# Kernel tuning notes

Hardware: AMD Instinct MI355X
Metric: run time of the kernel (lower is better)

## Reference

```python
import jax, jax.numpy as jnp
import numpy as np

NU = 100000  # user nodes
NI = 100000  # item nodes
D_IN = 128
D_OUT = 128
E = 800000   # edges per canonical etype


def setup_inputs() -> dict:
    key = jax.random.key(0)
    ks = jax.random.split(key, 14)
    s = 1.0 / np.sqrt(D_IN)
    return {
        "feat_user": jax.random.normal(ks[0], (NU, D_IN), jnp.float32),
        "feat_item": jax.random.normal(ks[1], (NI, D_IN), jnp.float32),
        "W_follows": jax.random.normal(ks[2], (D_OUT, D_IN), jnp.float32) * s,
        "b_follows": jax.random.normal(ks[3], (D_OUT,), jnp.float32) * s,
        "W_rates": jax.random.normal(ks[4], (D_OUT, D_IN), jnp.float32) * s,
        "b_rates": jax.random.normal(ks[5], (D_OUT,), jnp.float32) * s,
        "W_ratedby": jax.random.normal(ks[6], (D_OUT, D_IN), jnp.float32) * s,
        "b_ratedby": jax.random.normal(ks[7], (D_OUT,), jnp.float32) * s,
        "src_follows": jax.random.randint(ks[8], (E,), 0, NU),
        "dst_follows": jax.random.randint(ks[9], (E,), 0, NU),
        "src_rates": jax.random.randint(ks[10], (E,), 0, NU),
        "dst_rates": jax.random.randint(ks[11], (E,), 0, NI),
        "src_ratedby": jax.random.randint(ks[12], (E,), 0, NI),
        "dst_ratedby": jax.random.randint(ks[13], (E,), 0, NU),
    }


def _mean_agg(Wh, src, dst, n_dst):
    # gather transformed src features per edge, segment-mean over dst
    msg = Wh[src]  # [E, D_OUT]
    s = jax.ops.segment_sum(msg, dst, num_segments=n_dst)
    cnt = jax.ops.segment_sum(jnp.ones((dst.shape[0],), Wh.dtype), dst,
                              num_segments=n_dst)
    return s / jnp.maximum(cnt, 1.0)[:, None]  # zero-degree -> 0, like DGL


def reference(feat_user, feat_item, W_follows, b_follows, W_rates, b_rates,
              W_ratedby, b_ratedby, src_follows, dst_follows, src_rates,
              dst_rates, src_ratedby, dst_ratedby):
    # per-etype linear transform of source node features (Wh)
    Wh_f = feat_user @ W_follows.T + b_follows    # user -> user
    Wh_r = feat_user @ W_rates.T + b_rates        # user -> item
    Wh_rb = feat_item @ W_ratedby.T + b_ratedby   # item -> user
    # copy_u/mean per etype, then 'sum' combine across etypes per dst ntype
    h_user = (_mean_agg(Wh_f, src_follows, dst_follows, NU)
              + _mean_agg(Wh_rb, src_ratedby, dst_ratedby, NU))
    h_item = _mean_agg(Wh_r, src_rates, dst_rates, NI)
    return (h_user, h_item)
```

## Files before the change

### kernel.cpp

```cpp
#include <hip/hip_runtime.h>

#define NU 100000
#define NI 100000
#define DF 128
#define CAP 32
#define BCAP 768
#define NBKT 1600
#define CHUNK 4096

typedef __attribute__((ext_vector_type(8))) short bf16x8;
typedef __attribute__((ext_vector_type(4))) float f32x4;

__device__ __forceinline__ unsigned short f2bf(float f) {
    unsigned u = __float_as_uint(f);
    return (unsigned short)((u + 0x7fffu + ((u >> 16) & 1u)) >> 16);
}
__device__ __forceinline__ float bflo(unsigned v) { return __uint_as_float(v << 16); }
__device__ __forceinline__ float bfhi(unsigned v) { return __uint_as_float(v & 0xffff0000u); }

__global__ void wcvt_kernel(const float* __restrict__ W0,
                            const float* __restrict__ W1,
                            const float* __restrict__ W2,
                            unsigned short* __restrict__ out,
                            int* __restrict__ bcnt)
{
    const int i = blockIdx.x * 256 + threadIdx.x;
    if (i < 3 * 16384) {
        const float* src = (i < 16384) ? W0 : ((i < 32768) ? W1 : W2);
        out[i] = f2bf(src[i & 16383]);
    }
    if (i < 3 * NBKT * 16) bcnt[i] = 0;
}

__device__ __forceinline__ void load_afrag(const float* __restrict__ A,
                                           int row0, int q, int n, int M,
                                           bf16x8 afrag[2][4])
{
#pragma unroll
    for (int t = 0; t < 2; ++t) {
        const int rr = min(row0 + t * 16 + n, M - 1);
        const float* ap = A + (size_t)rr * DF + q * 8;
#pragma unroll
        for (int s = 0; s < 4; ++s) {
            const float4 f0 = *(const float4*)(ap + s * 32);
            const float4 f1 = *(const float4*)(ap + s * 32 + 4);
            bf16x8 fr;
            fr[0] = (short)f2bf(f0.x); fr[1] = (short)f2bf(f0.y);
            fr[2] = (short)f2bf(f0.z); fr[3] = (short)f2bf(f0.w);
            fr[4] = (short)f2bf(f1.x); fr[5] = (short)f2bf(f1.y);
            fr[6] = (short)f2bf(f1.z); fr[7] = (short)f2bf(f1.w);
            afrag[t][s] = fr;
        }
    }
}

__device__ __forceinline__ void mat_pass(const bf16x8 afrag[2][4],
                                         const unsigned short* __restrict__ Wbp,
                                         const float* __restrict__ bias,
                                         unsigned short* __restrict__ ot,
                                         int wv, int q, int n)
{
#pragma unroll 1
    for (int c = 0; c < 8; ++c) {
        const unsigned short* wp = Wbp + (size_t)(c * 16 + n) * DF + q * 8;
        bf16x8 bfrag[4];
#pragma unroll
        for (int s = 0; s < 4; ++s)
            bfrag[s] = *(const bf16x8*)(wp + s * 32);

        f32x4 acc0 = {0.f, 0.f, 0.f, 0.f};
        f32x4 acc1 = {0.f, 0.f, 0.f, 0.f};
#pragma unroll
        for (int s = 0; s < 4; ++s) {
            acc0 = __builtin_amdgcn_mfma_f32_16x16x32_bf16(afrag[0][s], bfrag[s], acc0, 0, 0, 0);
            acc1 = __builtin_amdgcn_mfma_f32_16x16x32_bf16(afrag[1][s], bfrag[s], acc1, 0, 0, 0);
        }

        const float bv = bias[c * 16 + n];
        const int col2 = (c * 16 + n) * 2;
#pragma unroll
        for (int i = 0; i < 4; ++i) {
            const int r0 = wv * 32 + q * 4 + i;
            const int swz = (r0 & 7) << 4;
            *(unsigned short*)((char*)ot + ((r0 * 256 + col2) ^ swz))       = f2bf(acc0[i] + bv);
            *(unsigned short*)((char*)ot + (((r0 + 16) * 256 + col2) ^ swz)) = f2bf(acc1[i] + bv);
        }
    }
}

__device__ __forceinline__ void flush_tile(const unsigned short* __restrict__ ot,
                                           unsigned short* __restrict__ Wh,
                                           int rowbase, int M, int tid)
{
    __syncthreads();
#pragma unroll
    for (int it = 0; it < 8; ++it) {
        const int chunk = it * 256 + tid;
        const int row = chunk >> 4;
        const int lbyte = chunk * 16;
        const uint4 v = *(const uint4*)((const char*)ot + (lbyte ^ ((row & 7) << 4)));
        if (rowbase + row < M)
            *(uint4*)((char*)Wh + (size_t)(rowbase + row) * 256 + (lbyte & 255)) = v;
    }
    __syncthreads();
}

__global__ __launch_bounds__(256)
void gemm3_kernel(const float* __restrict__ Au, const float* __restrict__ Ai,
                  const unsigned short* __restrict__ Wb,
                  const float* __restrict__ b_f, const float* __restrict__ b_r,
                  const float* __restrict__ b_rb,
                  unsigned short* __restrict__ Wh_f,
                  unsigned short* __restrict__ Wh_r,
                  unsigned short* __restrict__ Wh_rb, int M)
{
    __shared__ unsigned short ot[128 * 128];
    const int tid  = threadIdx.x;
    const int lane = tid & 63;
    const int wv   = tid >> 6;
    const int q    = lane >> 4;
    const int n    = lane & 15;
    const int row0 = blockIdx.x * 128 + wv * 32;

    bf16x8 afrag[2][4];
    load_afrag(Au, row0, q, n, M, afrag);
    mat_pass(afrag, Wb,             b_f, ot, wv, q, n);
    flush_tile(ot, Wh_f, blockIdx.x * 128, M, tid);
    mat_pass(afrag, Wb + 2 * 16384, b_r, ot, wv, q, n);
    flush_tile(ot, Wh_r, blockIdx.x * 128, M, tid);
    load_afrag(Ai, row0, q, n, M, afrag);
    mat_pass(afrag, Wb + 16384,     b_rb, ot, wv, q, n);
    flush_tile(ot, Wh_rb, blockIdx.x * 128, M, tid);
}

__global__ __launch_bounds__(256)
void bin3_kernel(const int* __restrict__ src0, const int* __restrict__ dst0, int n0, int nb0,
                 const int* __restrict__ src1, const int* __restrict__ dst1, int n1, int nb1,
                 const int* __restrict__ src2, const int* __restrict__ dst2, int n2,
                 int* __restrict__ bcnt, unsigned* __restrict__ pairs)
{
    __shared__ int hist[NBKT];
    const int tid = threadIdx.x;
    int b = blockIdx.x, e;
    const int* src; const int* dst; int n;
    if (b < nb0)            { e = 0; src = src0; dst = dst0; n = n0; }
    else if (b < nb0 + nb1) { b -= nb0; e = 1; src = src1; dst = dst1; n = n1; }
    else                    { b -= nb0 + nb1; e = 2; src = src2; dst = dst2; n = n2; }
    const int base = b * CHUNK;
    int* bc = bcnt + e * NBKT * 16;
    unsigned* pr = pairs + (size_t)e * NBKT * BCAP;

    for (int j = tid; j < NBKT; j += 256) hist[j] = 0;
    __syncthreads();

    unsigned pk[16];
    int meta[16];
#pragma unroll
    for (int k = 0; k < 16; ++k) {
        const int i = base + k * 256 + tid;
        if (i < n) {
            const unsigned d = (unsigned)dst[i];
            const unsigned s = (unsigned)src[i];
            pk[k] = (s << 6) | (d & 63u);
            const int p = atomicAdd(&hist[d >> 6], 1);
            meta[k] = (int)((d >> 6) << 16) | p;
        } else meta[k] = -1;
    }
    __syncthreads();
    for (int j = tid; j < NBKT; j += 256) {
        const int c = hist[j];
        hist[j] = (c > 0) ? atomicAdd(&bc[j * 16], c) : 0;
    }
    __syncthreads();
#pragma unroll
    for (int k = 0; k < 16; ++k) {
        if (meta[k] >= 0) {
            const int bkt = meta[k] >> 16;
            const int p = hist[bkt] + (meta[k] & 0xffff);
            if (p < BCAP) pr[(size_t)bkt * BCAP + p] = pk[k];
        }
    }
}

__device__ __forceinline__ void accum8(const uint4 u, float acc[8]) {
    acc[0] += bflo(u.x); acc[1] += bfhi(u.x);
    acc[2] += bflo(u.y); acc[3] += bfhi(u.y);
    acc[4] += bflo(u.z); acc[5] += bfhi(u.z);
    acc[6] += bflo(u.w); acc[7] += bfhi(u.w);
}

__device__ __forceinline__ void gather_q(const unsigned short* __restrict__ Wh,
                                         const unsigned* __restrict__ sl,
                                         int d, int qh, int c16, float acc[8])
{
    for (int j = 0; j < d; j += 8) {
        const int e0 = j + qh, e1 = j + 2 + qh, e2 = j + 4 + qh, e3 = j + 6 + qh;
        uint4 u0 = {0,0,0,0}, u1 = {0,0,0,0}, u2 = {0,0,0,0}, u3 = {0,0,0,0};
        if (e0 < d) u0 = *((const uint4*)(Wh + (size_t)sl[e0] * DF) + c16);
        if (e1 < d) u1 = *((const uint4*)(Wh + (size_t)sl[e1] * DF) + c16);
        if (e2 < d) u2 = *((const uint4*)(Wh + (size_t)sl[e2] * DF) + c16);
        if (e3 < d) u3 = *((const uint4*)(Wh + (size_t)sl[e3] * DF) + c16);
        accum8(u0, acc); accum8(u1, acc);
        accum8(u2, acc); accum8(u3, acc);
    }
}

__global__ __launch_bounds__(256, 8)
void bagg_kernel(const unsigned short* __restrict__ Wh_f,
                 const unsigned short* __restrict__ Wh_rb,
                 const unsigned short* __restrict__ Wh_r,
                 const int* __restrict__ bcnt, const unsigned* __restrict__ pairs,
                 float* __restrict__ out_user, float* __restrict__ out_item)
{
    __shared__ int cntA[64], cntB[64];
    __shared__ unsigned slotA[64 * CAP], slotB[64 * CAP];
    const int tid = threadIdx.x;
    const bool user = (blockIdx.x & 1) == 0;
    const int bkt = blockIdx.x >> 1;

    if (tid < 64) { cntA[tid] = 0; cntB[tid] = 0; }
    __syncthreads();

    const int wv = tid >> 6, lane = tid & 63;
    const int c16 = lane & 15;
    const int qh = (lane >> 4) & 1;
    const int h = lane >> 5;

    if (user) {
        const int nf  = min(bcnt[0 * NBKT * 16 + bkt * 16], BCAP);
        const int nrb = min(bcnt[1 * NBKT * 16 + bkt * 16], BCAP);
        const unsigned* prf  = pairs + (size_t)bkt * BCAP;
        const unsigned* prrb = pairs + (size_t)NBKT * BCAP + (size_t)bkt * BCAP;
        for (int i = tid; i < nf; i += 256) {
            const unsigned v = prf[i];
            const int dl = v & 63;
            const int p = atomicAdd(&cntA[dl], 1);
            if (p < CAP) slotA[dl * CAP + p] = v >> 6;
        }
        for (int i = tid; i < nrb; i += 256) {
            const unsigned v = prrb[i];
            const int dl = v & 63;
            const int p = atomicAdd(&cntB[dl], 1);
            if (p < CAP) slotB[dl * CAP + p] = v >> 6;
        }
        __syncthreads();

        for (int t = 0; t < 8; ++t) {
            const int dl = wv * 16 + t * 2 + h;
            const int node = bkt * 64 + dl;
            const int degf  = cntA[dl];
            const int degrb = cntB[dl];
            const int df  = min(degf, CAP);
            const int drb = min(degrb, CAP);

            float acc[8];
#pragma unroll
            for (int k = 0; k < 8; ++k) acc[k] = 0.f;
            gather_q(Wh_f, &slotA[dl * CAP], df, qh, c16, acc);
            const float invf = degf > 0 ? 1.f / (float)degf : 0.f;
            float res[8];
#pragma unroll
            for (int k = 0; k < 8; ++k) { res[k] = acc[k] * invf; acc[k] = 0.f; }

            gather_q(Wh_rb, &slotB[dl * CAP], drb, qh, c16, acc);
            const float invrb = degrb > 0 ? 1.f / (float)degrb : 0.f;
#pragma unroll
            for (int k = 0; k < 8; ++k) {
                res[k] += acc[k] * invrb;
                res[k] += __shfl_xor(res[k], 16, 64);
            }
            if (!(lane & 16) && node < NU) {
                float* op = out_user + (size_t)node * DF + c16 * 8;
                float4 o0 = {res[0], res[1], res[2], res[3]};
                float4 o1 = {res[4], res[5], res[6], res[7]};
                *(float4*)op = o0;
                *((float4*)op + 1) = o1;
            }
        }
    } else {
        const int nr = min(bcnt[2 * NBKT * 16 + bkt * 16], BCAP);
        const unsigned* prr = pairs + 2 * (size_t)NBKT * BCAP + (size_t)bkt * BCAP;
        for (int i = tid; i < nr; i += 256) {
            const unsigned v = prr[i];
            const int dl = v & 63;
            const int p = atomicAdd(&cntA[dl], 1);
            if (p < CAP) slotA[dl * CAP + p] = v >> 6;
        }
        __syncthreads();

        for (int t = 0; t < 8; ++t) {
            const int dl = wv * 16 + t * 2 + h;
            const int node = bkt * 64 + dl;
            const int degr = cntA[dl];
            const int dr = min(degr, CAP);

            float acc[8];
#pragma unroll
            for (int k = 0; k < 8; ++k) acc[k] = 0.f;
            gather_q(Wh_r, &slotA[dl * CAP], dr, qh, c16, acc);
            const float invr = degr > 0 ? 1.f / (float)degr : 0.f;
            float res[8];
#pragma unroll
            for (int k = 0; k < 8; ++k) {
                res[k] = acc[k] * invr;
                res[k] += __shfl_xor(res[k], 16, 64);
            }
            if (!(lane & 16) && node < NI) {
                float* op = out_item + (size_t)node * DF + c16 * 8;
                float4 o0 = {res[0], res[1], res[2], res[3]};
                float4 o1 = {res[4], res[5], res[6], res[7]};
                *(float4*)op = o0;
                *((float4*)op + 1) = o1;
            }
        }
    }
}

extern "C" void kernel_launch(void* const* d_in, const int* in_sizes, int n_in,
                              void* d_out, int out_size, void* d_ws,
                              size_t ws_size, hipStream_t stream)
{
    const float* feat_user = (const float*)d_in[0];
    const float* feat_item = (const float*)d_in[1];
    const float* W_f  = (const float*)d_in[2];
    const float* b_f  = (const float*)d_in[3];
    const float* W_r  = (const float*)d_in[4];
    const float* b_r  = (const float*)d_in[5];
    const float* W_rb = (const float*)d_in[6];
    const float* b_rb = (const float*)d_in[7];
    const int* src_f  = (const int*)d_in[8];
    const int* dst_f  = (const int*)d_in[9];
    const int* src_r  = (const int*)d_in[10];
    const int* dst_r  = (const int*)d_in[11];
    const int* src_rb = (const int*)d_in[12];
    const int* dst_rb = (const int*)d_in[13];
    const int Ef  = in_sizes[8];
    const int Er  = in_sizes[10];
    const int Erb = in_sizes[12];

    float* out_user = (float*)d_out;
    float* out_item = (float*)d_out + (size_t)NU * DF;

    char* p = (char*)d_ws;
    unsigned short* Wh_f  = (unsigned short*)p;  p += (size_t)NU * DF * 2;
    unsigned short* Wh_rb = (unsigned short*)p;  p += (size_t)NI * DF * 2;
    unsigned short* Wh_r  = (unsigned short*)p;  p += (size_t)NU * DF * 2;
    unsigned* pairs = (unsigned*)p;  p += 3 * (size_t)NBKT * BCAP * 4;
    int* bcnt = (int*)p;             p += 3 * (size_t)NBKT * 16 * 4;
    unsigned short* Wb = (unsigned short*)p;

    wcvt_kernel<<<300, 256, 0, stream>>>(W_f, W_rb, W_r, Wb, bcnt);

    gemm3_kernel<<<(NU + 127) / 128, 256, 0, stream>>>(
        feat_user, feat_item, Wb, b_f, b_r, b_rb, Wh_f, Wh_r, Wh_rb, NU);

    const int nb_f  = (Ef  + CHUNK - 1) / CHUNK;
    const int nb_rb = (Erb + CHUNK - 1) / CHUNK;
    const int nb_r  = (Er  + CHUNK - 1) / CHUNK;
    bin3_kernel<<<nb_f + nb_rb + nb_r, 256, 0, stream>>>(
        src_f,  dst_f,  Ef,  nb_f,
        src_rb, dst_rb, Erb, nb_rb,
        src_r,  dst_r,  Er,  bcnt, pairs);

    const int nbu = (NU + 63) / 64;
    bagg_kernel<<<2 * nbu, 256, 0, stream>>>(
        Wh_f, Wh_rb, Wh_r, bcnt, pairs, out_user, out_item);
}
```

Baseline: 409.5 us.

## Bin edges directly per node and co-schedule binning with GEMM blocks

Replaces the two-level bucket binning (block histogram, then per-bucket shared-memory regrouping inside the aggregation kernel) with direct per-node global atomic counters and slot arrays. The binning and GEMM kernels are fused into one launch whose blocks interleave, so edge binning overlaps the transform GEMM. The aggregation kernel then reads each node's slots straight from global memory, using wave shuffles to spread indices, and processes both user etypes in one interleaved loop. In exchange it issues one global atomic per edge on a larger counter array and writes a bigger slot buffer. The per-destination cap of 32 is unchanged, and the bucket-level overflow limit is gone.

```diff
diff --git a/kernel.cpp b/kernel.cpp
--- a/kernel.cpp
+++ b/kernel.cpp
@@ -4,12 +4,11 @@
 #define NI 100000
 #define DF 128
 #define CAP 32
-#define BCAP 768
-#define NBKT 1600
 #define CHUNK 4096
 
 typedef __attribute__((ext_vector_type(8))) short bf16x8;
 typedef __attribute__((ext_vector_type(4))) float f32x4;
+typedef __attribute__((ext_vector_type(2))) float f32x2;
 
 __device__ __forceinline__ unsigned short f2bf(float f) {
     unsigned u = __float_as_uint(f);
@@ -22,14 +21,14 @@
                             const float* __restrict__ W1,
                             const float* __restrict__ W2,
                             unsigned short* __restrict__ out,
-                            int* __restrict__ bcnt)
+                            int* __restrict__ cnt)
 {
     const int i = blockIdx.x * 256 + threadIdx.x;
     if (i < 3 * 16384) {
         const float* src = (i < 16384) ? W0 : ((i < 32768) ? W1 : W2);
         out[i] = f2bf(src[i & 16383]);
     }
-    if (i < 3 * NBKT * 16) bcnt[i] = 0;
+    if (i < 75000) ((int4*)cnt)[i] = make_int4(0, 0, 0, 0);
 }
 
 __device__ __forceinline__ void load_afrag(const float* __restrict__ A,
@@ -82,7 +81,7 @@
         for (int i = 0; i < 4; ++i) {
             const int r0 = wv * 32 + q * 4 + i;
             const int swz = (r0 & 7) << 4;
-            *(unsigned short*)((char*)ot + ((r0 * 256 + col2) ^ swz))       = f2bf(acc0[i] + bv);
+            *(unsigned short*)((char*)ot + ((r0 * 256 + col2) ^ swz))        = f2bf(acc0[i] + bv);
             *(unsigned short*)((char*)ot + (((r0 + 16) * 256 + col2) ^ swz)) = f2bf(acc1[i] + bv);
         }
     }
@@ -105,213 +104,195 @@
     __syncthreads();
 }
 
+__device__ __forceinline__ void bin_block(const int* __restrict__ src,
+                                          const int* __restrict__ dst, int n,
+                                          int lb, int* __restrict__ cnt_e,
+                                          unsigned* __restrict__ sl_e)
+{
+    const int base = lb * CHUNK;
+    const int tid = threadIdx.x;
+#pragma unroll
+    for (int k = 0; k < 16; k += 4) {
+        int d[4], s[4], ok[4];
+#pragma unroll
+        for (int u = 0; u < 4; ++u) {
+            const int i = base + (k + u) * 256 + tid;
+            ok[u] = (i < n);
+            const int ii = ok[u] ? i : 0;
+            d[u] = dst[ii]; s[u] = src[ii];
+        }
+#pragma unroll
+        for (int u = 0; u < 4; ++u) {
+            if (ok[u]) {
+                const int p = atomicAdd(&cnt_e[d[u]], 1);
+                if (p < CAP) sl_e[(size_t)d[u] * CAP + p] = (unsigned)s[u];
+            }
+        }
+    }
+}
+
 __global__ __launch_bounds__(256)
-void gemm3_kernel(const float* __restrict__ Au, const float* __restrict__ Ai,
-                  const unsigned short* __restrict__ Wb,
-                  const float* __restrict__ b_f, const float* __restrict__ b_r,
-                  const float* __restrict__ b_rb,
-                  unsigned short* __restrict__ Wh_f,
-                  unsigned short* __restrict__ Wh_r,
-                  unsigned short* __restrict__ Wh_rb, int M)
+void mid_kernel(const float* __restrict__ Au, const float* __restrict__ Ai,
+                const unsigned short* __restrict__ Wb,
+                const float* __restrict__ b_f, const float* __restrict__ b_r,
+                const float* __restrict__ b_rb,
+                unsigned short* __restrict__ Wh_f,
+                unsigned short* __restrict__ Wh_r,
+                unsigned short* __restrict__ Wh_rb, int M,
+                const int* __restrict__ src0, const int* __restrict__ dst0, int n0, int nb0,
+                const int* __restrict__ src1, const int* __restrict__ dst1, int n1, int nb1,
+                const int* __restrict__ src2, const int* __restrict__ dst2, int n2, int nbin,
+                int* __restrict__ cnt, unsigned* __restrict__ slots)
 {
     __shared__ unsigned short ot[128 * 128];
+    const int b = blockIdx.x;
+
+    if ((b & 1) && (b >> 1) < nbin) {
+        int lb = b >> 1;
+        if (lb < nb0) {
+            bin_block(src0, dst0, n0, lb, cnt, slots);
+        } else if (lb < nb0 + nb1) {
+            bin_block(src1, dst1, n1, lb - nb0, cnt + NU,
+                      slots + (size_t)NU * CAP);
+        } else {
+            bin_block(src2, dst2, n2, lb - nb0 - nb1, cnt + 2 * NU,
+                      slots + 2 * (size_t)NU * CAP);
+        }
+        return;
+    }
+
+    const int g = (b < 2 * nbin) ? (b >> 1) : (b - nbin);
     const int tid  = threadIdx.x;
     const int lane = tid & 63;
     const int wv   = tid >> 6;
     const int q    = lane >> 4;
     const int n    = lane & 15;
-    const int row0 = blockIdx.x * 128 + wv * 32;
+    const int row0 = g * 128 + wv * 32;
 
     bf16x8 afrag[2][4];
     load_afrag(Au, row0, q, n, M, afrag);
     mat_pass(afrag, Wb,             b_f, ot, wv, q, n);
-    flush_tile(ot, Wh_f, blockIdx.x * 128, M, tid);
+    flush_tile(ot, Wh_f, g * 128, M, tid);
     mat_pass(afrag, Wb + 2 * 16384, b_r, ot, wv, q, n);
-    flush_tile(ot, Wh_r, blockIdx.x * 128, M, tid);
+    flush_tile(ot, Wh_r, g * 128, M, tid);
     load_afrag(Ai, row0, q, n, M, afrag);
     mat_pass(afrag, Wb + 16384,     b_rb, ot, wv, q, n);
-    flush_tile(ot, Wh_rb, blockIdx.x * 128, M, tid);
+    flush_tile(ot, Wh_rb, g * 128, M, tid);
+}
+
+__device__ __forceinline__ void accum4(f32x2 acc[4], const uint4 u) {
+    acc[0] += (f32x2){bflo(u.x), bfhi(u.x)};
+    acc[1] += (f32x2){bflo(u.y), bfhi(u.y)};
+    acc[2] += (f32x2){bflo(u.z), bfhi(u.z)};
+    acc[3] += (f32x2){bflo(u.w), bfhi(u.w)};
 }
 
 __global__ __launch_bounds__(256)
-void bin3_kernel(const int* __restrict__ src0, const int* __restrict__ dst0, int n0, int nb0,
-                 const int* __restrict__ src1, const int* __restrict__ dst1, int n1, int nb1,
-                 const int* __restrict__ src2, const int* __restrict__ dst2, int n2,
-                 int* __restrict__ bcnt, unsigned* __restrict__ pairs)
-{
-    __shared__ int hist[NBKT];
-    const int tid = threadIdx.x;
-    int b = blockIdx.x, e;
-    const int* src; const int* dst; int n;
-    if (b < nb0)            { e = 0; src = src0; dst = dst0; n = n0; }
-    else if (b < nb0 + nb1) { b -= nb0; e = 1; src = src1; dst = dst1; n = n1; }
-    else                    { b -= nb0 + nb1; e = 2; src = src2; dst = dst2; n = n2; }
-    const int base = b * CHUNK;
-    int* bc = bcnt + e * NBKT * 16;
-    unsigned* pr = pairs + (size_t)e * NBKT * BCAP;
-
-    for (int j = tid; j < NBKT; j += 256) hist[j] = 0;
-    __syncthreads();
-
-    unsigned pk[16];
-    int meta[16];
-#pragma unroll
-    for (int k = 0; k < 16; ++k) {
-        const int i = base + k * 256 + tid;
-        if (i < n) {
-            const unsigned d = (unsigned)dst[i];
-            const unsigned s = (unsigned)src[i];
-            pk[k] = (s << 6) | (d & 63u);
-            const int p = atomicAdd(&hist[d >> 6], 1);
-            meta[k] = (int)((d >> 6) << 16) | p;
-        } else meta[k] = -1;
-    }
-    __syncthreads();
-    for (int j = tid; j < NBKT; j += 256) {
-        const int c = hist[j];
-        hist[j] = (c > 0) ? atomicAdd(&bc[j * 16], c) : 0;
-    }
-    __syncthreads();
-#pragma unroll
-    for (int k = 0; k < 16; ++k) {
-        if (meta[k] >= 0) {
-            const int bkt = meta[k] >> 16;
-            const int p = hist[bkt] + (meta[k] & 0xffff);
-            if (p < BCAP) pr[(size_t)bkt * BCAP + p] = pk[k];
-        }
-    }
-}
-
-__device__ __forceinline__ void accum8(const uint4 u, float acc[8]) {
-    acc[0] += bflo(u.x); acc[1] += bfhi(u.x);
-    acc[2] += bflo(u.y); acc[3] += bfhi(u.y);
-    acc[4] += bflo(u.z); acc[5] += bfhi(u.z);
-    acc[6] += bflo(u.w); acc[7] += bfhi(u.w);
-}
-
-__device__ __forceinline__ void gather_q(const unsigned short* __restrict__ Wh,
-                                         const unsigned* __restrict__ sl,
-                                         int d, int qh, int c16, float acc[8])
-{
-    for (int j = 0; j < d; j += 8) {
-        const int e0 = j + qh, e1 = j + 2 + qh, e2 = j + 4 + qh, e3 = j + 6 + qh;
-        uint4 u0 = {0,0,0,0}, u1 = {0,0,0,0}, u2 = {0,0,0,0}, u3 = {0,0,0,0};
-        if (e0 < d) u0 = *((const uint4*)(Wh + (size_t)sl[e0] * DF) + c16);
-        if (e1 < d) u1 = *((const uint4*)(Wh + (size_t)sl[e1] * DF) + c16);
-        if (e2 < d) u2 = *((const uint4*)(Wh + (size_t)sl[e2] * DF) + c16);
-        if (e3 < d) u3 = *((const uint4*)(Wh + (size_t)sl[e3] * DF) + c16);
-        accum8(u0, acc); accum8(u1, acc);
-        accum8(u2, acc); accum8(u3, acc);
-    }
-}
-
-__global__ __launch_bounds__(256, 8)
 void bagg_kernel(const unsigned short* __restrict__ Wh_f,
                  const unsigned short* __restrict__ Wh_rb,
                  const unsigned short* __restrict__ Wh_r,
-                 const int* __restrict__ bcnt, const unsigned* __restrict__ pairs,
+                 const int* __restrict__ cnt, const unsigned* __restrict__ slots,
                  float* __restrict__ out_user, float* __restrict__ out_item)
 {
-    __shared__ int cntA[64], cntB[64];
-    __shared__ unsigned slotA[64 * CAP], slotB[64 * CAP];
-    const int tid = threadIdx.x;
+    const int tid  = threadIdx.x;
+    const int wv   = tid >> 6, lane = tid & 63;
+    const int c16  = lane & 15;
+    const int qh   = (lane >> 4) & 1;
+    const int h    = lane >> 5;
+    const int sub  = lane & 31;
+    const int selb = lane & 32;
+
     const bool user = (blockIdx.x & 1) == 0;
-    const int bkt = blockIdx.x >> 1;
-
-    if (tid < 64) { cntA[tid] = 0; cntB[tid] = 0; }
-    __syncthreads();
-
-    const int wv = tid >> 6, lane = tid & 63;
-    const int c16 = lane & 15;
-    const int qh = (lane >> 4) & 1;
-    const int h = lane >> 5;
+    const int node = (blockIdx.x >> 1) * 8 + wv * 2 + h;
 
     if (user) {
-        const int nf  = min(bcnt[0 * NBKT * 16 + bkt * 16], BCAP);
-        const int nrb = min(bcnt[1 * NBKT * 16 + bkt * 16], BCAP);
-        const unsigned* prf  = pairs + (size_t)bkt * BCAP;
-        const unsigned* prrb = pairs + (size_t)NBKT * BCAP + (size_t)bkt * BCAP;
-        for (int i = tid; i < nf; i += 256) {
-            const unsigned v = prf[i];
-            const int dl = v & 63;
-            const int p = atomicAdd(&cntA[dl], 1);
-            if (p < CAP) slotA[dl * CAP + p] = v >> 6;
-        }
-        for (int i = tid; i < nrb; i += 256) {
-            const unsigned v = prrb[i];
-            const int dl = v & 63;
-            const int p = atomicAdd(&cntB[dl], 1);
-            if (p < CAP) slotB[dl * CAP + p] = v >> 6;
-        }
-        __syncthreads();
-
-        for (int t = 0; t < 8; ++t) {
-            const int dl = wv * 16 + t * 2 + h;
-            const int node = bkt * 64 + dl;
-            const int degf  = cntA[dl];
-            const int degrb = cntB[dl];
-            const int df  = min(degf, CAP);
-            const int drb = min(degrb, CAP);
-
-            float acc[8];
-#pragma unroll
-            for (int k = 0; k < 8; ++k) acc[k] = 0.f;
-            gather_q(Wh_f, &slotA[dl * CAP], df, qh, c16, acc);
-            const float invf = degf > 0 ? 1.f / (float)degf : 0.f;
-            float res[8];
-#pragma unroll
-            for (int k = 0; k < 8; ++k) { res[k] = acc[k] * invf; acc[k] = 0.f; }
-
-            gather_q(Wh_rb, &slotB[dl * CAP], drb, qh, c16, acc);
-            const float invrb = degrb > 0 ? 1.f / (float)degrb : 0.f;
-#pragma unroll
-            for (int k = 0; k < 8; ++k) {
-                res[k] += acc[k] * invrb;
-                res[k] += __shfl_xor(res[k], 16, 64);
-            }
-            if (!(lane & 16) && node < NU) {
-                float* op = out_user + (size_t)node * DF + c16 * 8;
-                float4 o0 = {res[0], res[1], res[2], res[3]};
-                float4 o1 = {res[4], res[5], res[6], res[7]};
-                *(float4*)op = o0;
-                *((float4*)op + 1) = o1;
-            }
+        const int degf  = cnt[node];
+        const int degrb = cnt[NU + node];
+        const int sf  = (int)slots[(size_t)node * CAP + sub];
+        const int srb = (int)slots[((size_t)NU + node) * CAP + sub];
+        const int df  = min(degf, CAP);
+        const int drb = min(degrb, CAP);
+        const int dmax = max(df, drb);
+
+        f32x2 accf[4], accrb[4];
+#pragma unroll
+        for (int k = 0; k < 4; ++k) { accf[k] = (f32x2){0.f, 0.f}; accrb[k] = (f32x2){0.f, 0.f}; }
+
+        for (int j = 0; j < dmax; j += 4) {
+            const int e0 = j + qh, e1 = j + 2 + qh;
+            const int if0 = __shfl(sf,  selb + e0, 64);
+            const int if1 = __shfl(sf,  selb + e1, 64);
+            const int ir0 = __shfl(srb, selb + e0, 64);
+            const int ir1 = __shfl(srb, selb + e1, 64);
+            uint4 a0 = {0,0,0,0}, a1 = {0,0,0,0}, r0 = {0,0,0,0}, r1 = {0,0,0,0};
+            if (e0 < df)  a0 = *((const uint4*)(Wh_f  + (size_t)if0 * DF) + c16);
+            if (e0 < drb) r0 = *((const uint4*)(Wh_rb + (size_t)ir0 * DF) + c16);
+            if (e1 < df)  a1 = *((const uint4*)(Wh_f  + (size_t)if1 * DF) + c16);
+            if (e1 < drb) r1 = *((const uint4*)(Wh_rb + (size_t)ir1 * DF) + c16);
+            accum4(accf, a0); accum4(accrb, r0);
+            accum4(accf, a1); accum4(accrb, r1);
+        }
+
+        const float invf  = degf  > 0 ? 1.f / (float)degf  : 0.f;
+        const float invrb = degrb > 0 ? 1.f / (float)degrb : 0.f;
+        const f32x2 vf = {invf, invf}, vrb = {invrb, invrb};
+        float res[8];
+#pragma unroll
+        for (int k = 0; k < 4; ++k) {
+            const f32x2 r = accf[k] * vf + accrb[k] * vrb;
+            res[2 * k]     = r.x;
+            res[2 * k + 1] = r.y;
+        }
+#pragma unroll
+        for (int k = 0; k < 8; ++k) res[k] += __shfl_xor(res[k], 16, 64);
+        if (!(lane & 16)) {
+            float* op = out_user + (size_t)node * DF + c16 * 8;
+            float4 o0 = {res[0], res[1], res[2], res[3]};
+            float4 o1 = {res[4], res[5], res[6], res[7]};
+            *(float4*)op = o0;
+            *((float4*)op + 1) = o1;
         }
     } else {
-        const int nr = min(bcnt[2 * NBKT * 16 + bkt * 16], BCAP);
-        const unsigned* prr = pairs + 2 * (size_t)NBKT * BCAP + (size_t)bkt * BCAP;
-        for (int i = tid; i < nr; i += 256) {
-            const unsigned v = prr[i];
-            const int dl = v & 63;
-            const int p = atomicAdd(&cntA[dl], 1);
-            if (p < CAP) slotA[dl * CAP + p] = v >> 6;
-        }
-        __syncthreads();
-
-        for (int t = 0; t < 8; ++t) {
-            const int dl = wv * 16 + t * 2 + h;
-            const int node = bkt * 64 + dl;
-            const int degr = cntA[dl];
-            const int dr = min(degr, CAP);
-
-            float acc[8];
-#pragma unroll
-            for (int k = 0; k < 8; ++k) acc[k] = 0.f;
-            gather_q(Wh_r, &slotA[dl * CAP], dr, qh, c16, acc);
-            const float invr = degr > 0 ? 1.f / (float)degr : 0.f;
-            float res[8];
-#pragma unroll
-            for (int k = 0; k < 8; ++k) {
-                res[k] = acc[k] * invr;
-                res[k] += __shfl_xor(res[k], 16, 64);
-            }
-            if (!(lane & 16) && node < NI) {
-                float* op = out_item + (size_t)node * DF + c16 * 8;
-                float4 o0 = {res[0], res[1], res[2], res[3]};
-                float4 o1 = {res[4], res[5], res[6], res[7]};
-                *(float4*)op = o0;
-                *((float4*)op + 1) = o1;
-            }
+        const int degr = cnt[2 * NU + node];
+        const int sr = (int)slots[(2 * (size_t)NU + node) * CAP + sub];
+        const int dr = min(degr, CAP);
+
+        f32x2 acc[4];
+#pragma unroll
+        for (int k = 0; k < 4; ++k) acc[k] = (f32x2){0.f, 0.f};
+
+        for (int j = 0; j < dr; j += 8) {
+            const int e0 = j + qh, e1 = j + 2 + qh, e2 = j + 4 + qh, e3 = j + 6 + qh;
+            const int i0 = __shfl(sr, selb + e0, 64);
+            const int i1 = __shfl(sr, selb + e1, 64);
+            const int i2 = __shfl(sr, selb + e2, 64);
+            const int i3 = __shfl(sr, selb + e3, 64);
+            uint4 u0 = {0,0,0,0}, u1 = {0,0,0,0}, u2 = {0,0,0,0}, u3 = {0,0,0,0};
+            if (e0 < dr) u0 = *((const uint4*)(Wh_r + (size_t)i0 * DF) + c16);
+            if (e1 < dr) u1 = *((const uint4*)(Wh_r + (size_t)i1 * DF) + c16);
+            if (e2 < dr) u2 = *((const uint4*)(Wh_r + (size_t)i2 * DF) + c16);
+            if (e3 < dr) u3 = *((const uint4*)(Wh_r + (size_t)i3 * DF) + c16);
+            accum4(acc, u0); accum4(acc, u1);
+            accum4(acc, u2); accum4(acc, u3);
+        }
+
+        const float invr = degr > 0 ? 1.f / (float)degr : 0.f;
+        const f32x2 vr = {invr, invr};
+        float res[8];
+#pragma unroll
+        for (int k = 0; k < 4; ++k) {
+            const f32x2 r = acc[k] * vr;
+            res[2 * k]     = r.x;
+            res[2 * k + 1] = r.y;
+        }
+#pragma unroll
+        for (int k = 0; k < 8; ++k) res[k] += __shfl_xor(res[k], 16, 64);
+        if (!(lane & 16)) {
+            float* op = out_item + (size_t)node * DF + c16 * 8;
+            float4 o0 = {res[0], res[1], res[2], res[3]};
+            float4 o1 = {res[4], res[5], res[6], res[7]};
+            *(float4*)op = o0;
+            *((float4*)op + 1) = o1;
         }
     }
 }
@@ -345,24 +326,24 @@
     unsigned short* Wh_f  = (unsigned short*)p;  p += (size_t)NU * DF * 2;
     unsigned short* Wh_rb = (unsigned short*)p;  p += (size_t)NI * DF * 2;
     unsigned short* Wh_r  = (unsigned short*)p;  p += (size_t)NU * DF * 2;
-    unsigned* pairs = (unsigned*)p;  p += 3 * (size_t)NBKT * BCAP * 4;
-    int* bcnt = (int*)p;             p += 3 * (size_t)NBKT * 16 * 4;
+    unsigned* slots = (unsigned*)p;  p += 3 * (size_t)NU * CAP * 4;
+    int* cnt = (int*)p;              p += 3 * (size_t)NU * 4;
     unsigned short* Wb = (unsigned short*)p;
 
-    wcvt_kernel<<<300, 256, 0, stream>>>(W_f, W_rb, W_r, Wb, bcnt);
-
-    gemm3_kernel<<<(NU + 127) / 128, 256, 0, stream>>>(
-        feat_user, feat_item, Wb, b_f, b_r, b_rb, Wh_f, Wh_r, Wh_rb, NU);
+    wcvt_kernel<<<300, 256, 0, stream>>>(W_f, W_rb, W_r, Wb, cnt);
 
     const int nb_f  = (Ef  + CHUNK - 1) / CHUNK;
     const int nb_rb = (Erb + CHUNK - 1) / CHUNK;
     const int nb_r  = (Er  + CHUNK - 1) / CHUNK;
-    bin3_kernel<<<nb_f + nb_rb + nb_r, 256, 0, stream>>>(
+    const int nbin  = nb_f + nb_rb + nb_r;
+    const int ngemm = (NU + 127) / 128;
+    mid_kernel<<<ngemm + nbin, 256, 0, stream>>>(
+        feat_user, feat_item, Wb, b_f, b_r, b_rb, Wh_f, Wh_r, Wh_rb, NU,
         src_f,  dst_f,  Ef,  nb_f,
         src_rb, dst_rb, Erb, nb_rb,
-        src_r,  dst_r,  Er,  bcnt, pairs);
-
-    const int nbu = (NU + 63) / 64;
-    bagg_kernel<<<2 * nbu, 256, 0, stream>>>(
-        Wh_f, Wh_rb, Wh_r, bcnt, pairs, out_user, out_item);
-}
+        src_r,  dst_r,  Er,  nbin,
+        cnt, slots);
+
+    bagg_kernel<<<2 * (NU / 8), 256, 0, stream>>>(
+        Wh_f, Wh_rb, Wh_r, cnt, slots, out_user, out_item);
+}
```

Result: slower. 440.4 us (+7.5%).

## Stage GEMM A-tile through LDS and shuffle-broadcast gather slot indices

Applied to the files above, without the earlier changes.

The GEMM kernel now loads each 128-row fp32 input tile with coalesced float4 reads, converts it to bf16 into swizzled LDS, and builds MFMA A-fragments from LDS, replacing strided per-lane global loads. The gather kernel loads each node's slot list into registers once and broadcasts the indices with wave shuffles instead of reading LDS per edge. It also reduces the gather unroll from 4 to 2 loads per iteration, which may lower memory-level parallelism, and the shuffle loop runs to the larger degree of the two half-waves.

```diff
diff --git a/kernel.cpp b/kernel.cpp
--- a/kernel.cpp
+++ b/kernel.cpp
@@ -32,25 +32,34 @@
     if (i < 3 * NBKT * 16) bcnt[i] = 0;
 }
 
-__device__ __forceinline__ void load_afrag(const float* __restrict__ A,
-                                           int row0, int q, int n, int M,
-                                           bf16x8 afrag[2][4])
+__device__ __forceinline__ void stage_a(const float* __restrict__ A,
+                                        int rowbase, int M,
+                                        unsigned short* __restrict__ lds, int tid)
+{
+#pragma unroll
+    for (int it = 0; it < 16; ++it) {
+        const int idx = it * 256 + tid;
+        const int row = idx >> 5;
+        const int c4  = idx & 31;
+        const int rr  = min(rowbase + row, M - 1);
+        const float4 f = *(const float4*)(A + (size_t)rr * DF + c4 * 4);
+        ushort4 h;
+        h.x = f2bf(f.x); h.y = f2bf(f.y); h.z = f2bf(f.z); h.w = f2bf(f.w);
+        *(ushort4*)((char*)lds + ((row * 256 + c4 * 8) ^ ((row & 7) << 4))) = h;
+    }
+}
+
+__device__ __forceinline__ void frag_from_lds(const unsigned short* __restrict__ lds,
+                                              int wv, int q, int n,
+                                              bf16x8 afrag[2][4])
 {
 #pragma unroll
     for (int t = 0; t < 2; ++t) {
-        const int rr = min(row0 + t * 16 + n, M - 1);
-        const float* ap = A + (size_t)rr * DF + q * 8;
-#pragma unroll
-        for (int s = 0; s < 4; ++s) {
-            const float4 f0 = *(const float4*)(ap + s * 32);
-            const float4 f1 = *(const float4*)(ap + s * 32 + 4);
-            bf16x8 fr;
-            fr[0] = (short)f2bf(f0.x); fr[1] = (short)f2bf(f0.y);
-            fr[2] = (short)f2bf(f0.z); fr[3] = (short)f2bf(f0.w);
-            fr[4] = (short)f2bf(f1.x); fr[5] = (short)f2bf(f1.y);
-            fr[6] = (short)f2bf(f1.z); fr[7] = (short)f2bf(f1.w);
-            afrag[t][s] = fr;
-        }
+        const int row = wv * 32 + t * 16 + n;
+#pragma unroll
+        for (int s = 0; s < 4; ++s)
+            afrag[t][s] = *(const bf16x8*)((const char*)lds +
+                ((row * 256 + q * 16 + s * 64) ^ ((row & 7) << 4)));
     }
 }
 
@@ -82,7 +91,7 @@
         for (int i = 0; i < 4; ++i) {
             const int r0 = wv * 32 + q * 4 + i;
             const int swz = (r0 & 7) << 4;
-            *(unsigned short*)((char*)ot + ((r0 * 256 + col2) ^ swz))       = f2bf(acc0[i] + bv);
+            *(unsigned short*)((char*)ot + ((r0 * 256 + col2) ^ swz))        = f2bf(acc0[i] + bv);
             *(unsigned short*)((char*)ot + (((r0 + 16) * 256 + col2) ^ swz)) = f2bf(acc1[i] + bv);
         }
     }
@@ -114,23 +123,30 @@
                   unsigned short* __restrict__ Wh_r,
                   unsigned short* __restrict__ Wh_rb, int M)
 {
-    __shared__ unsigned short ot[128 * 128];
+    __shared__ unsigned short lds[128 * 128];
     const int tid  = threadIdx.x;
     const int lane = tid & 63;
     const int wv   = tid >> 6;
     const int q    = lane >> 4;
     const int n    = lane & 15;
-    const int row0 = blockIdx.x * 128 + wv * 32;
+    const int rowbase = blockIdx.x * 128;
 
     bf16x8 afrag[2][4];
-    load_afrag(Au, row0, q, n, M, afrag);
-    mat_pass(afrag, Wb,             b_f, ot, wv, q, n);
-    flush_tile(ot, Wh_f, blockIdx.x * 128, M, tid);
-    mat_pass(afrag, Wb + 2 * 16384, b_r, ot, wv, q, n);
-    flush_tile(ot, Wh_r, blockIdx.x * 128, M, tid);
-    load_afrag(Ai, row0, q, n, M, afrag);
-    mat_pass(afrag, Wb + 16384,     b_rb, ot, wv, q, n);
-    flush_tile(ot, Wh_rb, blockIdx.x * 128, M, tid);
+    stage_a(Au, rowbase, M, lds, tid);
+    __syncthreads();
+    frag_from_lds(lds, wv, q, n, afrag);
+    __syncthreads();
+    mat_pass(afrag, Wb,             b_f, lds, wv, q, n);
+    flush_tile(lds, Wh_f, rowbase, M, tid);
+    mat_pass(afrag, Wb + 2 * 16384, b_r, lds, wv, q, n);
+    flush_tile(lds, Wh_r, rowbase, M, tid);
+
+    stage_a(Ai, rowbase, M, lds, tid);
+    __syncthreads();
+    frag_from_lds(lds, wv, q, n, afrag);
+    __syncthreads();
+    mat_pass(afrag, Wb + 16384,     b_rb, lds, wv, q, n);
+    flush_tile(lds, Wh_rb, rowbase, M, tid);
 }
 
 __global__ __launch_bounds__(256)
@@ -190,18 +206,17 @@
 }
 
 __device__ __forceinline__ void gather_q(const unsigned short* __restrict__ Wh,
-                                         const unsigned* __restrict__ sl,
-                                         int d, int qh, int c16, float acc[8])
-{
-    for (int j = 0; j < d; j += 8) {
-        const int e0 = j + qh, e1 = j + 2 + qh, e2 = j + 4 + qh, e3 = j + 6 + qh;
-        uint4 u0 = {0,0,0,0}, u1 = {0,0,0,0}, u2 = {0,0,0,0}, u3 = {0,0,0,0};
-        if (e0 < d) u0 = *((const uint4*)(Wh + (size_t)sl[e0] * DF) + c16);
-        if (e1 < d) u1 = *((const uint4*)(Wh + (size_t)sl[e1] * DF) + c16);
-        if (e2 < d) u2 = *((const uint4*)(Wh + (size_t)sl[e2] * DF) + c16);
-        if (e3 < d) u3 = *((const uint4*)(Wh + (size_t)sl[e3] * DF) + c16);
-        accum8(u0, acc); accum8(u1, acc);
-        accum8(u2, acc); accum8(u3, acc);
+                                         int s, int d, int dmax,
+                                         int selbase, int qh, int c16,
+                                         float acc[8])
+{
+    for (int j = 0; j < dmax; j += 4) {
+        const int e0 = j + qh;
+        const int e1 = j + 2 + qh;
+        const int id0 = __shfl(s, selbase + e0, 64);
+        const int id1 = __shfl(s, selbase + e1, 64);
+        if (e0 < d) accum8(*((const uint4*)(Wh + (size_t)id0 * DF) + c16), acc);
+        if (e1 < d) accum8(*((const uint4*)(Wh + (size_t)id1 * DF) + c16), acc);
     }
 }
 
@@ -225,6 +240,7 @@
     const int c16 = lane & 15;
     const int qh = (lane >> 4) & 1;
     const int h = lane >> 5;
+    const int selbase = lane & 32;
 
     if (user) {
         const int nf  = min(bcnt[0 * NBKT * 16 + bkt * 16], BCAP);
@@ -250,19 +266,23 @@
             const int node = bkt * 64 + dl;
             const int degf  = cntA[dl];
             const int degrb = cntB[dl];
+            const int sf  = (int)slotA[dl * CAP + (lane & 31)];
+            const int srb = (int)slotB[dl * CAP + (lane & 31)];
             const int df  = min(degf, CAP);
             const int drb = min(degrb, CAP);
+            const int dfm  = max(df,  __shfl_xor(df, 32, 64));
+            const int drbm = max(drb, __shfl_xor(drb, 32, 64));
 
             float acc[8];
 #pragma unroll
             for (int k = 0; k < 8; ++k) acc[k] = 0.f;
-            gather_q(Wh_f, &slotA[dl * CAP], df, qh, c16, acc);
+            gather_q(Wh_f, sf, df, dfm, selbase, qh, c16, acc);
             const float invf = degf > 0 ? 1.f / (float)degf : 0.f;
             float res[8];
 #pragma unroll
             for (int k = 0; k < 8; ++k) { res[k] = acc[k] * invf; acc[k] = 0.f; }
 
-            gather_q(Wh_rb, &slotB[dl * CAP], drb, qh, c16, acc);
+            gather_q(Wh_rb, srb, drb, drbm, selbase, qh, c16, acc);
             const float invrb = degrb > 0 ? 1.f / (float)degrb : 0.f;
 #pragma unroll
             for (int k = 0; k < 8; ++k) {
@@ -292,12 +312,14 @@
             const int dl = wv * 16 + t * 2 + h;
             const int node = bkt * 64 + dl;
             const int degr = cntA[dl];
+            const int sr = (int)slotA[dl * CAP + (lane & 31)];
             const int dr = min(degr, CAP);
+            const int drm = max(dr, __shfl_xor(dr, 32, 64));
 
             float acc[8];
 #pragma unroll
             for (int k = 0; k < 8; ++k) acc[k] = 0.f;
-            gather_q(Wh_r, &slotA[dl * CAP], dr, qh, c16, acc);
+            gather_q(Wh_r, sr, dr, drm, selbase, qh, c16, acc);
             const float invr = degr > 0 ? 1.f / (float)degr : 0.f;
             float res[8];
 #pragma unroll
```

After: 423.1 us. +3.3%, slower.
